# Kernel optimization log

Measured on AMD Instinct MI355X. Metric: run time of the kernel, lower is better.

Reference implementation:

```python
import jax, jax.numpy as jnp
import numpy as np

N = 100000   # num_nodes
E = 1250000  # num_edges
D = 64       # embedding_dim
L = 3        # num_layers


def setup_inputs() -> dict:
    key = jax.random.key(0)
    k1, k2, k3, k4 = jax.random.split(key, 4)
    edge_index = jax.random.randint(k1, (2, E), 0, N, dtype=jnp.int64)
    edge_label_index = jax.random.randint(k2, (2, E), 0, N, dtype=jnp.int64)
    # xavier_uniform init of Embedding(N, D)
    bound = float(np.sqrt(6.0 / (N + D)))
    emb_weight = jax.random.uniform(k3, (N, D), jnp.float32, -bound, bound)
    alpha = jnp.full((L + 1,), 1.0 / (L + 1), dtype=jnp.float32)
    return {"edge_index": edge_index, "edge_label_index": edge_label_index,
            "emb_weight": emb_weight, "alpha": alpha}


def reference(edge_index, edge_label_index, emb_weight, alpha):
    src, dst = edge_index[0], edge_index[1]
    n = emb_weight.shape[0]
    # gcn_norm (LGConv, no self-loops): deg over destination, sym normalization
    deg = jax.ops.segment_sum(jnp.ones(src.shape[0], emb_weight.dtype), dst, num_segments=n)
    dis = jnp.where(deg > 0, jax.lax.rsqrt(jnp.where(deg > 0, deg, 1.0)), 0.0)
    w = dis[src] * dis[dst]  # [E]

    weights = jax.nn.softmax(alpha)  # [L+1]
    x = emb_weight
    out = x * weights[0]
    for i in range(L):
        # LGConv: out[dst] += norm * x[src]
        x = jax.ops.segment_sum(w[:, None] * x[src], dst, num_segments=n)
        out = out + x * weights[i + 1]

    # predict_link_embedding: per-edge dot product
    return (out[edge_label_index[0]] * out[edge_label_index[1]]).sum(axis=-1)
```

## Files before the change

### kernel.cpp

```cpp
#include <hip/hip_runtime.h>
#include <math.h>

#define DIM 64
#define PART_T 4096
#define BK_SHIFT 9
#define BK_SPAN 512
#define BK_CAP 8192
#define BK_PAD 2048
#define BK_REG (BK_CAP + BK_PAD)

typedef _Float16 half8 __attribute__((ext_vector_type(8)));


__device__ __forceinline__ half8 shfl_xor_h8(half8 v, int mask) {
    int4 iv;
    __builtin_memcpy(&iv, &v, 16);
    iv.x = __shfl_xor(iv.x, mask, 64);
    iv.y = __shfl_xor(iv.y, mask, 64);
    iv.z = __shfl_xor(iv.z, mask, 64);
    iv.w = __shfl_xor(iv.w, mask, 64);
    half8 r;
    __builtin_memcpy(&r, &iv, 16);
    return r;
}

__device__ __forceinline__ half8 dpp_ror8_h8(half8 v) {
    int4 iv;
    __builtin_memcpy(&iv, &v, 16);
    int4 r;
    r.x = __builtin_amdgcn_update_dpp(0, iv.x, 0x128, 0xF, 0xF, true);
    r.y = __builtin_amdgcn_update_dpp(0, iv.y, 0x128, 0xF, 0xF, true);
    r.z = __builtin_amdgcn_update_dpp(0, iv.z, 0x128, 0xF, 0xF, true);
    r.w = __builtin_amdgcn_update_dpp(0, iv.w, 0x128, 0xF, 0xF, true);
    half8 out;
    __builtin_memcpy(&out, &r, 16);
    return out;
}

__device__ __forceinline__ float dpp_sum8_f32(float v) {
    int x = __float_as_int(v);
    v += __int_as_float(__builtin_amdgcn_update_dpp(0, x, 0xB1, 0xF, 0xF, true));
    x = __float_as_int(v);
    v += __int_as_float(__builtin_amdgcn_update_dpp(0, x, 0x4E, 0xF, 0xF, true));
    x = __float_as_int(v);
    v += __int_as_float(__builtin_amdgcn_update_dpp(0, x, 0x141, 0xF, 0xF, true));
    return v;
}

__device__ __forceinline__ int wave_incl_scan(int v) {
    int lane = threadIdx.x & 63;
    #pragma unroll
    for (int d = 1; d < 64; d <<= 1) {
        int n = __shfl_up(v, d, 64);
        if (lane >= d) v += n;
    }
    return v;
}

__device__ __forceinline__ int block_scan_excl(int v, int* wsum) {
    int incl = wave_incl_scan(v);
    int w = threadIdx.x >> 6;
    if ((threadIdx.x & 63) == 63) wsum[w] = incl;
    __syncthreads();
    int offset = 0;
    #pragma unroll
    for (int i = 0; i < 3; ++i) offset += (i < w) ? wsum[i] : 0;
    return offset + incl - v;
}


__global__ void init_kernel(int* __restrict__ gcursor, int K) {
    int t = threadIdx.x;
    if (t < K) gcursor[t] = t * BK_CAP;
}


__global__ void part_kernel(const int* __restrict__ src, const int* __restrict__ dst,
                            int* __restrict__ gcursor, unsigned int* __restrict__ part,
                            int E, int K) {
    __shared__ unsigned int tmp_rec[PART_T];
    __shared__ unsigned int reord[PART_T];
    __shared__ unsigned char tmp_bkt[PART_T];
    __shared__ unsigned char tmp_bkt2[PART_T];
    __shared__ int hist[256];
    __shared__ int lstart[256];
    __shared__ int cursor[256];
    __shared__ int gbase[256];
    __shared__ int wsum[4];
    int t = threadIdx.x;
    int tile = blockIdx.x * PART_T;
    int n = E - tile; if (n > PART_T) n = PART_T;

    hist[t] = 0;
    __syncthreads();

    for (int i = t; i < n; i += 256) {
        int s = src[tile + i];
        int d = dst[tile + i];
        int b = d >> BK_SHIFT;
        tmp_rec[i] = (unsigned int)s | ((unsigned int)(d & (BK_SPAN - 1)) << 17);
        tmp_bkt[i] = (unsigned char)b;
        atomicAdd(&hist[b], 1);
    }
    __syncthreads();

    int hv = hist[t];
    int excl = block_scan_excl(hv, wsum);
    lstart[t] = excl;
    cursor[t] = excl;
    if (t < K && hv > 0) gbase[t] = atomicAdd(&gcursor[t], hv);
    __syncthreads();

    for (int i = t; i < n; i += 256) {
        int b = tmp_bkt[i];
        int r = atomicAdd(&cursor[b], 1);
        reord[r] = tmp_rec[i];
        tmp_bkt2[r] = (unsigned char)b;
    }
    __syncthreads();

    for (int i = t; i < n; i += 256) {
        int b = tmp_bkt2[i];
        part[gbase[b] + (i - lstart[b])] = reord[i];
    }
}


__global__ void csr_kernel(const unsigned int* __restrict__ part, const int* __restrict__ gcursor,
                           int2* __restrict__ prange, int* __restrict__ csr_src,
                           float* __restrict__ dis, int N) {
    __shared__ int h[BK_SPAN];
    __shared__ int pfx[BK_SPAN + 1];
    __shared__ int wsum[4];
    int b = blockIdx.x;
    int t = threadIdx.x;
    int pbase = b * BK_CAP;
    int cnt   = gcursor[b] - pbase;
    int qbase = b * BK_REG;
    int nodeBase = b << BK_SHIFT;

    h[t] = 0; h[t + 256] = 0;
    __syncthreads();

    for (int j = t; j < cnt; j += 256) {
        unsigned int rec = part[pbase + j];
        atomicAdd(&h[rec >> 17], 1);
    }
    __syncthreads();

    int d0 = h[2 * t], d1 = h[2 * t + 1];
    {
        int i0 = nodeBase + 2 * t, i1 = i0 + 1;
        if (i0 < N) dis[i0] = d0 > 0 ? 1.0f / sqrtf((float)d0) : 0.0f;
        if (i1 < N) dis[i1] = d1 > 0 ? 1.0f / sqrtf((float)d1) : 0.0f;
    }
    int p0 = (d0 + 3) & ~3;
    int p1 = (d1 + 3) & ~3;
    int excl = block_scan_excl(p0 + p1, wsum);
    pfx[2 * t]     = excl;
    pfx[2 * t + 1] = excl + p0;
    h[2 * t]       = excl;
    h[2 * t + 1]   = excl + p0;
    if (t == 255) pfx[BK_SPAN] = excl + p0 + p1;
    __syncthreads();

    #pragma unroll
    for (int k = 0; k < 2; ++k) {
        int i = t + k * 256;
        int idx = nodeBase + i;
        if (idx < N) prange[idx] = make_int2(qbase + pfx[i], qbase + pfx[i + 1]);
    }
    __syncthreads();

    for (int j = t; j < cnt; j += 256) {
        unsigned int rec = part[pbase + j];
        int dl = (int)(rec >> 17);
        int s  = (int)(rec & 0x1FFFFu);
        int p = atomicAdd(&h[dl], 1);
        csr_src[qbase + p] = s;
    }
    __syncthreads();

    #pragma unroll
    for (int k = 0; k < 2; ++k) {
        int i = t + k * 256;
        int endp = pfx[i + 1];
        for (int p = h[i]; p < endp; ++p) csr_src[qbase + p] = N;
    }
}


__global__ void conv_kernel(const float* __restrict__ emb, const float* __restrict__ dis,
                            half8* __restrict__ g0, half8* __restrict__ g1,
                            half8* __restrict__ g2, int n8, int N) {
    int i = blockIdx.x * blockDim.x + threadIdx.x;
    if (i < 8) {
        half8 z = (half8)(_Float16)0;
        g0[(size_t)N * 8 + i] = z;
        g1[(size_t)N * 8 + i] = z;
        g2[(size_t)N * 8 + i] = z;
    }
    if (i >= n8) return;
    int v = i >> 3;
    float d = dis[v];
    const float4* e4 = (const float4*)emb;
    float4 a = e4[2 * i], b = e4[2 * i + 1];
    half8 h;
    h[0] = (_Float16)(d * a.x); h[1] = (_Float16)(d * a.y);
    h[2] = (_Float16)(d * a.z); h[3] = (_Float16)(d * a.w);
    h[4] = (_Float16)(d * b.x); h[5] = (_Float16)(d * b.y);
    h[6] = (_Float16)(d * b.z); h[7] = (_Float16)(d * b.w);
    g0[i] = h;
}


__device__ __forceinline__ void softmax4(const float* __restrict__ alpha, float* w) {
    float a0 = alpha[0], a1 = alpha[1], a2 = alpha[2], a3 = alpha[3];
    float m = fmaxf(fmaxf(a0, a1), fmaxf(a2, a3));
    float e0 = expf(a0 - m), e1 = expf(a1 - m), e2 = expf(a2 - m), e3 = expf(a3 - m);
    float s = 1.0f / (e0 + e1 + e2 + e3);
    w[0] = e0 * s; w[1] = e1 * s; w[2] = e2 * s; w[3] = e3 * s;
}

__global__ void spmm_kernel(const int2* __restrict__ prange, const int* __restrict__ csr_src,
                            const float* __restrict__ dis,
                            const half8* __restrict__ gin, half8* __restrict__ gout, int N) {
    int lane = threadIdx.x & 63;
    int wave = blockIdx.x * (blockDim.x >> 6) + (threadIdx.x >> 6);
    int v = wave * 2 + (lane >> 5);
    int slot = (lane >> 3) & 3;
    int sub  = lane & 7;
    bool valid = v < N;
    int beg = 0, end = 0;
    if (valid) { int2 pr = prange[v]; beg = pr.x; end = pr.y; }
    const int4* csr4 = (const int4*)csr_src;
    half8 acc0 = (half8)(_Float16)0;
    half8 acc1 = (half8)(_Float16)0;
    for (int j = beg + slot * 4; j < end; j += 16) {
        int4 c = csr4[j >> 2];
        acc0 = acc0 + gin[c.x * 8 + sub];
        acc1 = acc1 + gin[c.y * 8 + sub];
        acc0 = acc0 + gin[c.z * 8 + sub];
        acc1 = acc1 + gin[c.w * 8 + sub];
    }
    half8 acc = acc0 + acc1;
    acc = acc + dpp_ror8_h8(acc);
    acc = acc + shfl_xor_h8(acc, 16);
    if (valid && (lane & 31) < 8) {
        float d = dis[v];
        float d2 = d * d;
        half8 o;
        #pragma unroll
        for (int k = 0; k < 8; ++k) o[k] = (_Float16)(d2 * (float)acc[k]);
        gout[v * 8 + sub] = o;
    }
}

__global__ void spmm_final_kernel(const int2* __restrict__ prange, const int* __restrict__ csr_src,
                                  const float* __restrict__ dis,
                                  const float* __restrict__ emb, const half8* __restrict__ g1,
                                  const half8* __restrict__ g2, half8* __restrict__ out,
                                  const float* __restrict__ alpha, int N) {
    int lane = threadIdx.x & 63;
    int wave = blockIdx.x * (blockDim.x >> 6) + (threadIdx.x >> 6);
    int v = wave * 2 + (lane >> 5);
    int slot = (lane >> 3) & 3;
    int sub  = lane & 7;
    bool valid = v < N;
    int beg = 0, end = 0;
    if (valid) { int2 pr = prange[v]; beg = pr.x; end = pr.y; }
    const int4* csr4 = (const int4*)csr_src;
    half8 acc0 = (half8)(_Float16)0;
    half8 acc1 = (half8)(_Float16)0;
    for (int j = beg + slot * 4; j < end; j += 16) {
        int4 c = csr4[j >> 2];
        acc0 = acc0 + g2[c.x * 8 + sub];
        acc1 = acc1 + g2[c.y * 8 + sub];
        acc0 = acc0 + g2[c.z * 8 + sub];
        acc1 = acc1 + g2[c.w * 8 + sub];
    }
    half8 acc = acc0 + acc1;
    acc = acc + dpp_ror8_h8(acc);
    acc = acc + shfl_xor_h8(acc, 16);
    if (valid && (lane & 31) < 8) {
        float w[4];
        softmax4(alpha, w);
        float d  = dis[v];
        float iv = d > 0.0f ? 1.0f / d : 0.0f;
        const float4* e4 = (const float4*)emb;
        float4 ea = e4[v * 16 + sub * 2];
        float4 eb = e4[v * 16 + sub * 2 + 1];
        half8 h1 = g1[v * 8 + sub];
        half8 h2 = g2[v * 8 + sub];
        float ef[8] = {ea.x, ea.y, ea.z, ea.w, eb.x, eb.y, eb.z, eb.w};
        half8 o;
        #pragma unroll
        for (int k = 0; k < 8; ++k) {
            float x1 = (float)h1[k] * iv;
            float x2 = (float)h2[k] * iv;
            float x3 = d * (float)acc[k];
            float val = w[0] * ef[k] + w[1] * x1 + w[2] * x2 + w[3] * x3;
            o[k] = (_Float16)val;
        }
        out[v * 8 + sub] = o;
    }
}

__global__ void dot_kernel(const int* __restrict__ a, const int* __restrict__ b,
                           const half8* __restrict__ out, float* __restrict__ res, int E) {
    long long g = (long long)blockIdx.x * blockDim.x + threadIdx.x;
    int e   = (int)(g >> 3);
    int sub = (int)(g & 7);
    if (e >= E) return;
    int ia = a[e];
    int ib = b[e];
    half8 va = out[ia * 8 + sub];
    half8 vb = out[ib * 8 + sub];
#if __has_builtin(__builtin_amdgcn_fdot2)
    float v = 0.f;
    v = __builtin_amdgcn_fdot2(__builtin_shufflevector(va, va, 0, 1),
                               __builtin_shufflevector(vb, vb, 0, 1), v, false);
    v = __builtin_amdgcn_fdot2(__builtin_shufflevector(va, va, 2, 3),
                               __builtin_shufflevector(vb, vb, 2, 3), v, false);
    v = __builtin_amdgcn_fdot2(__builtin_shufflevector(va, va, 4, 5),
                               __builtin_shufflevector(vb, vb, 4, 5), v, false);
    v = __builtin_amdgcn_fdot2(__builtin_shufflevector(va, va, 6, 7),
                               __builtin_shufflevector(vb, vb, 6, 7), v, false);
#else
    float v = 0.f;
    #pragma unroll
    for (int k = 0; k < 8; ++k) v += (float)va[k] * (float)vb[k];
#endif
    v = dpp_sum8_f32(v);
    if (sub == 0) res[e] = v;
}


static inline size_t align256(size_t x) { return (x + 255) & ~(size_t)255; }

extern "C" void kernel_launch(void* const* d_in, const int* in_sizes, int n_in,
                              void* d_out, int out_size, void* d_ws, size_t ws_size,
                              hipStream_t stream) {
    const int* edge_index = (const int*)d_in[0];
    const int* edge_label = (const int*)d_in[1];
    const float* emb      = (const float*)d_in[2];
    const float* alpha    = (const float*)d_in[3];

    const int E = in_sizes[0] / 2;
    const int N = in_sizes[2] / DIM;
    const int K = (N + BK_SPAN - 1) >> BK_SHIFT;

    const int* src = edge_index;
    const int* dst = edge_index + E;
    const int* la  = edge_label;
    const int* lb  = edge_label + E;

    char* ws = (char*)d_ws;
    size_t off = 0;
    float* dis     = (float*)(ws + off); off = align256(off + (size_t)N * 4);
    int2*  prange  = (int2*)(ws + off);  off = align256(off + (size_t)N * 8);
    int*   gcursor = (int*)(ws + off);   off = align256(off + (size_t)256 * 4);
    unsigned int* part = (unsigned int*)(ws + off); off = align256(off + (size_t)K * BK_CAP * 4);
    int*   csr_src = (int*)(ws + off);   off = align256(off + (size_t)K * BK_REG * 4);
    half8* g0      = (half8*)(ws + off); off = align256(off + (size_t)(N + 1) * DIM * 2);
    half8* g1      = (half8*)(ws + off); off = align256(off + (size_t)(N + 1) * DIM * 2);
    half8* g2      = (half8*)(ws + off); off = align256(off + (size_t)(N + 1) * DIM * 2);
    half8* outbuf  = g0;
    (void)ws_size;

    const int B = 256;
    const int gridT = (E + PART_T - 1) / PART_T;

    init_kernel<<<1, B, 0, stream>>>(gcursor, K);

    part_kernel<<<gridT, B, 0, stream>>>(src, dst, gcursor, part, E, K);

    csr_kernel<<<K, B, 0, stream>>>(part, gcursor, prange, csr_src, dis, N);

    const int n8 = N * DIM / 8;
    conv_kernel<<<(n8 + B - 1) / B, B, 0, stream>>>(emb, dis, g0, g1, g2, n8, N);

    const int nodesPerBlock = (B / 64) * 2;
    const int gridS = (N + nodesPerBlock - 1) / nodesPerBlock;
    spmm_kernel<<<gridS, B, 0, stream>>>(prange, csr_src, dis, g0, g1, N);
    spmm_kernel<<<gridS, B, 0, stream>>>(prange, csr_src, dis, g1, g2, N);
    spmm_final_kernel<<<gridS, B, 0, stream>>>(prange, csr_src, dis, emb, g1, g2,
                                               outbuf, alpha, N);

    const long long dthreads = (long long)E * 8;
    const int gridD = (int)((dthreads + B - 1) / B);
    dot_kernel<<<gridD, B, 0, stream>>>(la, lb, outbuf, (float*)d_out, E);
}
```

Measured before the change: 230.0 us.

## Split feature dimension into four column planes to shrink gather working set

Feature buffers are reorganised into four planes of 16 fp16 columns each (32 bytes per node per plane), and the SpMM kernels process one plane per block group. Each node gets 8 lanes (4 edge slots × 2 subvectors) instead of 32, and the reduction uses two DPP steps. The aim is for each plane's gather footprint (~3.2MB) to fit better in cache, raising hit rates for the random neighbour gathers. The dot product is split into four passes that accumulate into the output. This costs extra passes over the CSR indices and label indices, plus read-modify-write traffic on the result array.

```diff
diff --git a/kernel.cpp b/kernel.cpp
--- a/kernel.cpp
+++ b/kernel.cpp
@@ -12,39 +12,18 @@
 typedef _Float16 half8 __attribute__((ext_vector_type(8)));
 
 
-__device__ __forceinline__ half8 shfl_xor_h8(half8 v, int mask) {
-    int4 iv;
-    __builtin_memcpy(&iv, &v, 16);
-    iv.x = __shfl_xor(iv.x, mask, 64);
-    iv.y = __shfl_xor(iv.y, mask, 64);
-    iv.z = __shfl_xor(iv.z, mask, 64);
-    iv.w = __shfl_xor(iv.w, mask, 64);
-    half8 r;
-    __builtin_memcpy(&r, &iv, 16);
-    return r;
-}
-
-__device__ __forceinline__ half8 dpp_ror8_h8(half8 v) {
+template<int CTRL>
+__device__ __forceinline__ half8 dpp_h8(half8 v) {
     int4 iv;
     __builtin_memcpy(&iv, &v, 16);
     int4 r;
-    r.x = __builtin_amdgcn_update_dpp(0, iv.x, 0x128, 0xF, 0xF, true);
-    r.y = __builtin_amdgcn_update_dpp(0, iv.y, 0x128, 0xF, 0xF, true);
-    r.z = __builtin_amdgcn_update_dpp(0, iv.z, 0x128, 0xF, 0xF, true);
-    r.w = __builtin_amdgcn_update_dpp(0, iv.w, 0x128, 0xF, 0xF, true);
+    r.x = __builtin_amdgcn_update_dpp(0, iv.x, CTRL, 0xF, 0xF, true);
+    r.y = __builtin_amdgcn_update_dpp(0, iv.y, CTRL, 0xF, 0xF, true);
+    r.z = __builtin_amdgcn_update_dpp(0, iv.z, CTRL, 0xF, 0xF, true);
+    r.w = __builtin_amdgcn_update_dpp(0, iv.w, CTRL, 0xF, 0xF, true);
     half8 out;
     __builtin_memcpy(&out, &r, 16);
     return out;
-}
-
-__device__ __forceinline__ float dpp_sum8_f32(float v) {
-    int x = __float_as_int(v);
-    v += __int_as_float(__builtin_amdgcn_update_dpp(0, x, 0xB1, 0xF, 0xF, true));
-    x = __float_as_int(v);
-    v += __int_as_float(__builtin_amdgcn_update_dpp(0, x, 0x4E, 0xF, 0xF, true));
-    x = __float_as_int(v);
-    v += __int_as_float(__builtin_amdgcn_update_dpp(0, x, 0x141, 0xF, 0xF, true));
-    return v;
 }
 
 __device__ __forceinline__ int wave_incl_scan(int v) {
@@ -192,16 +171,19 @@
 
 __global__ void conv_kernel(const float* __restrict__ emb, const float* __restrict__ dis,
                             half8* __restrict__ g0, half8* __restrict__ g1,
-                            half8* __restrict__ g2, int n8, int N) {
+                            half8* __restrict__ g2, int N, size_t pstride) {
     int i = blockIdx.x * blockDim.x + threadIdx.x;
     if (i < 8) {
+        int q = i >> 1, s = i & 1;
         half8 z = (half8)(_Float16)0;
-        g0[(size_t)N * 8 + i] = z;
-        g1[(size_t)N * 8 + i] = z;
-        g2[(size_t)N * 8 + i] = z;
-    }
-    if (i >= n8) return;
+        g0[q * pstride + (size_t)N * 2 + s] = z;
+        g1[q * pstride + (size_t)N * 2 + s] = z;
+        g2[q * pstride + (size_t)N * 2 + s] = z;
+    }
+    if (i >= N * 8) return;
     int v = i >> 3;
+    int c = i & 7;
+    int q = c >> 1, s = c & 1;
     float d = dis[v];
     const float4* e4 = (const float4*)emb;
     float4 a = e4[2 * i], b = e4[2 * i + 1];
@@ -210,7 +192,7 @@
     h[2] = (_Float16)(d * a.z); h[3] = (_Float16)(d * a.w);
     h[4] = (_Float16)(d * b.x); h[5] = (_Float16)(d * b.y);
     h[6] = (_Float16)(d * b.z); h[7] = (_Float16)(d * b.w);
-    g0[i] = h;
+    g0[q * pstride + (size_t)v * 2 + s] = h;
 }
 
 
@@ -224,35 +206,37 @@
 
 __global__ void spmm_kernel(const int2* __restrict__ prange, const int* __restrict__ csr_src,
                             const float* __restrict__ dis,
-                            const half8* __restrict__ gin, half8* __restrict__ gout, int N) {
+                            const half8* __restrict__ gin, half8* __restrict__ gout,
+                            int N, int gpq, size_t pstride) {
+    int q  = blockIdx.x / gpq;
+    int bq = blockIdx.x % gpq;
     int lane = threadIdx.x & 63;
-    int wave = blockIdx.x * (blockDim.x >> 6) + (threadIdx.x >> 6);
-    int v = wave * 2 + (lane >> 5);
-    int slot = (lane >> 3) & 3;
-    int sub  = lane & 7;
+    int wave = bq * (blockDim.x >> 6) + (threadIdx.x >> 6);
+    int v = wave * 8 + (lane >> 3);
+    int sub  = (lane >> 2) & 1;
+    int slot = lane & 3;
     bool valid = v < N;
     int beg = 0, end = 0;
     if (valid) { int2 pr = prange[v]; beg = pr.x; end = pr.y; }
+    const half8* gq = gin + (size_t)q * pstride;
     const int4* csr4 = (const int4*)csr_src;
-    half8 acc0 = (half8)(_Float16)0;
-    half8 acc1 = (half8)(_Float16)0;
+    half8 acc = (half8)(_Float16)0;
     for (int j = beg + slot * 4; j < end; j += 16) {
         int4 c = csr4[j >> 2];
-        acc0 = acc0 + gin[c.x * 8 + sub];
-        acc1 = acc1 + gin[c.y * 8 + sub];
-        acc0 = acc0 + gin[c.z * 8 + sub];
-        acc1 = acc1 + gin[c.w * 8 + sub];
-    }
-    half8 acc = acc0 + acc1;
-    acc = acc + dpp_ror8_h8(acc);
-    acc = acc + shfl_xor_h8(acc, 16);
-    if (valid && (lane & 31) < 8) {
+        acc = acc + gq[(size_t)c.x * 2 + sub];
+        acc = acc + gq[(size_t)c.y * 2 + sub];
+        acc = acc + gq[(size_t)c.z * 2 + sub];
+        acc = acc + gq[(size_t)c.w * 2 + sub];
+    }
+    acc = acc + dpp_h8<0xB1>(acc);
+    acc = acc + dpp_h8<0x4E>(acc);
+    if (valid && (lane & 3) == 0) {
         float d = dis[v];
         float d2 = d * d;
         half8 o;
         #pragma unroll
         for (int k = 0; k < 8; ++k) o[k] = (_Float16)(d2 * (float)acc[k]);
-        gout[v * 8 + sub] = o;
+        gout[(size_t)q * pstride + (size_t)v * 2 + sub] = o;
     }
 }
 
@@ -260,38 +244,40 @@
                                   const float* __restrict__ dis,
                                   const float* __restrict__ emb, const half8* __restrict__ g1,
                                   const half8* __restrict__ g2, half8* __restrict__ out,
-                                  const float* __restrict__ alpha, int N) {
+                                  const float* __restrict__ alpha, int N, int gpq,
+                                  size_t pstride) {
+    int q  = blockIdx.x / gpq;
+    int bq = blockIdx.x % gpq;
     int lane = threadIdx.x & 63;
-    int wave = blockIdx.x * (blockDim.x >> 6) + (threadIdx.x >> 6);
-    int v = wave * 2 + (lane >> 5);
-    int slot = (lane >> 3) & 3;
-    int sub  = lane & 7;
+    int wave = bq * (blockDim.x >> 6) + (threadIdx.x >> 6);
+    int v = wave * 8 + (lane >> 3);
+    int sub  = (lane >> 2) & 1;
+    int slot = lane & 3;
     bool valid = v < N;
     int beg = 0, end = 0;
     if (valid) { int2 pr = prange[v]; beg = pr.x; end = pr.y; }
+    const half8* g2q = g2 + (size_t)q * pstride;
     const int4* csr4 = (const int4*)csr_src;
-    half8 acc0 = (half8)(_Float16)0;
-    half8 acc1 = (half8)(_Float16)0;
+    half8 acc = (half8)(_Float16)0;
     for (int j = beg + slot * 4; j < end; j += 16) {
         int4 c = csr4[j >> 2];
-        acc0 = acc0 + g2[c.x * 8 + sub];
-        acc1 = acc1 + g2[c.y * 8 + sub];
-        acc0 = acc0 + g2[c.z * 8 + sub];
-        acc1 = acc1 + g2[c.w * 8 + sub];
-    }
-    half8 acc = acc0 + acc1;
-    acc = acc + dpp_ror8_h8(acc);
-    acc = acc + shfl_xor_h8(acc, 16);
-    if (valid && (lane & 31) < 8) {
+        acc = acc + g2q[(size_t)c.x * 2 + sub];
+        acc = acc + g2q[(size_t)c.y * 2 + sub];
+        acc = acc + g2q[(size_t)c.z * 2 + sub];
+        acc = acc + g2q[(size_t)c.w * 2 + sub];
+    }
+    acc = acc + dpp_h8<0xB1>(acc);
+    acc = acc + dpp_h8<0x4E>(acc);
+    if (valid && (lane & 3) == 0) {
         float w[4];
         softmax4(alpha, w);
         float d  = dis[v];
         float iv = d > 0.0f ? 1.0f / d : 0.0f;
         const float4* e4 = (const float4*)emb;
-        float4 ea = e4[v * 16 + sub * 2];
-        float4 eb = e4[v * 16 + sub * 2 + 1];
-        half8 h1 = g1[v * 8 + sub];
-        half8 h2 = g2[v * 8 + sub];
+        float4 ea = e4[(size_t)v * 16 + q * 4 + sub * 2];
+        float4 eb = e4[(size_t)v * 16 + q * 4 + sub * 2 + 1];
+        half8 h1 = g1[(size_t)q * pstride + (size_t)v * 2 + sub];
+        half8 h2 = g2q[(size_t)v * 2 + sub];
         float ef[8] = {ea.x, ea.y, ea.z, ea.w, eb.x, eb.y, eb.z, eb.w};
         half8 o;
         #pragma unroll
@@ -302,20 +288,22 @@
             float val = w[0] * ef[k] + w[1] * x1 + w[2] * x2 + w[3] * x3;
             o[k] = (_Float16)val;
         }
-        out[v * 8 + sub] = o;
+        out[(size_t)q * pstride + (size_t)v * 2 + sub] = o;
     }
 }
 
 __global__ void dot_kernel(const int* __restrict__ a, const int* __restrict__ b,
-                           const half8* __restrict__ out, float* __restrict__ res, int E) {
+                           const half8* __restrict__ outp, float* __restrict__ res,
+                           int E, int q, int first, size_t pstride) {
     long long g = (long long)blockIdx.x * blockDim.x + threadIdx.x;
-    int e   = (int)(g >> 3);
-    int sub = (int)(g & 7);
+    int e   = (int)(g >> 1);
+    int sub = (int)(g & 1);
     if (e >= E) return;
     int ia = a[e];
     int ib = b[e];
-    half8 va = out[ia * 8 + sub];
-    half8 vb = out[ib * 8 + sub];
+    const half8* op = outp + (size_t)q * pstride;
+    half8 va = op[(size_t)ia * 2 + sub];
+    half8 vb = op[(size_t)ib * 2 + sub];
 #if __has_builtin(__builtin_amdgcn_fdot2)
     float v = 0.f;
     v = __builtin_amdgcn_fdot2(__builtin_shufflevector(va, va, 0, 1),
@@ -331,8 +319,11 @@
     #pragma unroll
     for (int k = 0; k < 8; ++k) v += (float)va[k] * (float)vb[k];
 #endif
-    v = dpp_sum8_f32(v);
-    if (sub == 0) res[e] = v;
+    v += __shfl_xor(v, 1, 64);
+    if (sub == 0) {
+        if (first) res[e] = v;
+        else       res[e] += v;
+    }
 }
 
 
@@ -355,6 +346,8 @@
     const int* la  = edge_label;
     const int* lb  = edge_label + E;
 
+    const size_t pstride = (size_t)(N + 1) * 2;
+
     char* ws = (char*)d_ws;
     size_t off = 0;
     float* dis     = (float*)(ws + off); off = align256(off + (size_t)N * 4);
@@ -362,9 +355,9 @@
     int*   gcursor = (int*)(ws + off);   off = align256(off + (size_t)256 * 4);
     unsigned int* part = (unsigned int*)(ws + off); off = align256(off + (size_t)K * BK_CAP * 4);
     int*   csr_src = (int*)(ws + off);   off = align256(off + (size_t)K * BK_REG * 4);
-    half8* g0      = (half8*)(ws + off); off = align256(off + (size_t)(N + 1) * DIM * 2);
-    half8* g1      = (half8*)(ws + off); off = align256(off + (size_t)(N + 1) * DIM * 2);
-    half8* g2      = (half8*)(ws + off); off = align256(off + (size_t)(N + 1) * DIM * 2);
+    half8* g0      = (half8*)(ws + off); off = align256(off + pstride * 4 * 16);
+    half8* g1      = (half8*)(ws + off); off = align256(off + pstride * 4 * 16);
+    half8* g2      = (half8*)(ws + off); off = align256(off + pstride * 4 * 16);
     half8* outbuf  = g0;
     (void)ws_size;
 
@@ -377,17 +370,20 @@
 
     csr_kernel<<<K, B, 0, stream>>>(part, gcursor, prange, csr_src, dis, N);
 
-    const int n8 = N * DIM / 8;
-    conv_kernel<<<(n8 + B - 1) / B, B, 0, stream>>>(emb, dis, g0, g1, g2, n8, N);
-
-    const int nodesPerBlock = (B / 64) * 2;
-    const int gridS = (N + nodesPerBlock - 1) / nodesPerBlock;
-    spmm_kernel<<<gridS, B, 0, stream>>>(prange, csr_src, dis, g0, g1, N);
-    spmm_kernel<<<gridS, B, 0, stream>>>(prange, csr_src, dis, g1, g2, N);
-    spmm_final_kernel<<<gridS, B, 0, stream>>>(prange, csr_src, dis, emb, g1, g2,
-                                               outbuf, alpha, N);
-
-    const long long dthreads = (long long)E * 8;
+    conv_kernel<<<(N * 8 + B - 1) / B, B, 0, stream>>>(emb, dis, g0, g1, g2, N, pstride);
+
+    const int nodesPerBlock = (B / 64) * 8;
+    const int gpq = (N + nodesPerBlock - 1) / nodesPerBlock;
+    spmm_kernel<<<gpq * 4, B, 0, stream>>>(prange, csr_src, dis, g0, g1, N, gpq, pstride);
+    spmm_kernel<<<gpq * 4, B, 0, stream>>>(prange, csr_src, dis, g1, g2, N, gpq, pstride);
+    spmm_final_kernel<<<gpq * 4, B, 0, stream>>>(prange, csr_src, dis, emb, g1, g2,
+                                                 outbuf, alpha, N, gpq, pstride);
+
+    const long long dthreads = (long long)E * 2;
     const int gridD = (int)((dthreads + B - 1) / B);
-    dot_kernel<<<gridD, B, 0, stream>>>(la, lb, outbuf, (float*)d_out, E);
-}
+    float* res = (float*)d_out;
+    dot_kernel<<<gridD, B, 0, stream>>>(la, lb, outbuf, res, E, 0, 1, pstride);
+    dot_kernel<<<gridD, B, 0, stream>>>(la, lb, outbuf, res, E, 1, 0, pstride);
+    dot_kernel<<<gridD, B, 0, stream>>>(la, lb, outbuf, res, E, 2, 0, pstride);
+    dot_kernel<<<gridD, B, 0, stream>>>(la, lb, outbuf, res, E, 3, 0, pstride);
+}
```

Measured after the change: 303.4 us. 1.32x slower.
